# Optimization experiments

Hardware: AMD Instinct MI355X
Metric: run time of the kernel (lower is better)

The kernel has to match this reference:

```python
import jax, jax.numpy as jnp
import numpy as np

N_NODES = 50000
N_EDGES = 600000
IN_DIM = 128
HID_DIM = 128


def setup_inputs() -> dict:
    key = jax.random.key(0)
    k_h, k_src, k_dst, k_w1, k_b1, k_w2, k_b2 = jax.random.split(key, 7)
    h = jax.random.normal(k_h, (N_NODES, IN_DIM), dtype=jnp.float32)
    src = jax.random.randint(k_src, (N_EDGES,), 0, N_NODES, dtype=jnp.int32)
    dst = jax.random.randint(k_dst, (N_EDGES,), 0, N_NODES, dtype=jnp.int32)
    # Edge MLP params: Linear(in_dim, out_dim) -> ReLU -> Linear(out_dim, 1) -> ReLU
    s1 = 1.0 / np.sqrt(IN_DIM)
    s2 = 1.0 / np.sqrt(HID_DIM)
    W1 = jax.random.uniform(k_w1, (IN_DIM, HID_DIM), jnp.float32, -s1, s1)
    b1 = jax.random.uniform(k_b1, (HID_DIM,), jnp.float32, -s1, s1)
    W2 = jax.random.uniform(k_w2, (HID_DIM, 1), jnp.float32, -s2, s2)
    b2 = jax.random.uniform(k_b2, (1,), jnp.float32, -s2, s2)
    return {"h": h, "src": src, "dst": dst, "W1": W1, "b1": b1, "W2": W2, "b2": b2}


def reference(h, src, dst, W1, b1, W2, b2):
    n_nodes = h.shape[0]
    # Edge MLP on feature differences (gather src/dst node features)
    dif = h[src] - h[dst]                                   # [E, D]
    hidden = jax.nn.relu(dif @ W1 + b1)                      # [E, H]
    att = jax.nn.relu(hidden @ W2 + b2)[:, 0]                # [E]
    att = jax.nn.sigmoid(att)                                # [E]
    # EdgeWeightNorm('right') on reversed graph: divide by the sum of
    # attention weights over edges sharing the same ORIGINAL source node.
    denom = jax.ops.segment_sum(att, src, num_segments=n_nodes)  # [N]
    w = att / denom[src]                                     # [E]
    # Message: w_e * src features, sum-aggregated at destination nodes
    msg = w[:, None] * h[src]                                # [E, D]
    out = jax.ops.segment_sum(msg, dst, num_segments=n_nodes)  # [N, D]
    return out
```

## Files before the change

kernel.cpp:

```cpp
#include <hip/hip_runtime.h>


typedef unsigned int uint;
typedef unsigned short ushort;
typedef __attribute__((ext_vector_type(8))) short short8;
typedef __attribute__((ext_vector_type(4))) float f32x4;
typedef __attribute__((ext_vector_type(2))) _Float16 h2;

static __device__ __forceinline__ uint pack_f16(float a, float b) {
  _Float16 ha = (_Float16)a, hb = (_Float16)b;
  unsigned short ua = __builtin_bit_cast(unsigned short, ha);
  unsigned short ub = __builtin_bit_cast(unsigned short, hb);
  return ((uint)ub << 16) | ua;
}
static __device__ __forceinline__ float2 unpack_f16(uint u) {
  _Float16 lo = __builtin_bit_cast(_Float16, (unsigned short)(u & 0xffffu));
  _Float16 hi = __builtin_bit_cast(_Float16, (unsigned short)(u >> 16));
  return make_float2((float)lo, (float)hi);
}
static __device__ __forceinline__ h2 as_h2(uint u) { return __builtin_bit_cast(h2, u); }
static __device__ __forceinline__ h2 relu2(h2 a) {
  h2 r;
  r.x = a.x > (_Float16)0 ? a.x : (_Float16)0;
  r.y = a.y > (_Float16)0 ? a.y : (_Float16)0;
  return r;
}
static __device__ __forceinline__ float dot2acc(h2 a, h2 b, float c) {
#if __has_builtin(__builtin_amdgcn_fdot2)
  return __builtin_amdgcn_fdot2(a, b, c, false);
#else
  return c + (float)a.x * (float)b.x + (float)a.y * (float)b.y;
#endif
}
static __device__ __forceinline__ ushort f2bf(float x) {
  uint u = __float_as_uint(x);
  u += 0x7fffu + ((u >> 16) & 1u);
  return (ushort)(u >> 16);
}

__global__ __launch_bounds__(256) void k_misc(const float* __restrict__ W1,
                                              ushort* __restrict__ w1t_swz,
                                              const int* __restrict__ dst,
                                              int* __restrict__ counts, int n_edges) {
  int b = blockIdx.x;
  if (b < 64) {
    int idx = b * 256 + threadIdx.x;
    int n = idx >> 7, k = idx & 127;
    float v = W1[k * 128 + n];
    int byte_off = n * 256 + ((k * 2) ^ ((n & 7) << 4));
    w1t_swz[byte_off >> 1] = f2bf(v);
  } else {
    int i = (b - 64) * 256 + threadIdx.x;
    int stride = (gridDim.x - 64) * 256;
    for (int e = i; e < n_edges; e += stride) atomicAdd(&counts[dst[e]], 1);
  }
}

__global__ __launch_bounds__(256) void k_gemm(const float* __restrict__ h,
                                              const ushort* __restrict__ w1t_swz,
                                              uint* __restrict__ gh,
                                              uint4* __restrict__ hh4,
                                              int n_nodes) {
  __shared__ ushort w1s[16384];
  int tid = threadIdx.x;
  {
    const uint4* srcw = (const uint4*)w1t_swz;
    uint4* dstw = (uint4*)w1s;
    #pragma unroll
    for (int i = 0; i < 8; ++i) dstw[tid + 256 * i] = srcw[tid + 256 * i];
  }
  __syncthreads();
  int wave = tid >> 6, lane = tid & 63;
  int tile = blockIdx.x * 4 + wave;
  if (tile * 16 >= n_nodes) return;
  int n0 = tile * 16;
  int l15 = lane & 15, kq = lane >> 4;
  int row = n0 + l15;

  f32x4 acc[8];
  #pragma unroll
  for (int ct = 0; ct < 8; ++ct) acc[ct] = (f32x4){0.f, 0.f, 0.f, 0.f};

  #pragma unroll
  for (int kb = 0; kb < 4; ++kb) {
    const float* hp = &h[(size_t)row * 128 + kb * 32 + kq * 8];
    float4 p0 = *(const float4*)hp;
    float4 p1 = *(const float4*)(hp + 4);
    short8 a;
    a[0] = (short)f2bf(p0.x); a[1] = (short)f2bf(p0.y);
    a[2] = (short)f2bf(p0.z); a[3] = (short)f2bf(p0.w);
    a[4] = (short)f2bf(p1.x); a[5] = (short)f2bf(p1.y);
    a[6] = (short)f2bf(p1.z); a[7] = (short)f2bf(p1.w);
    uint4 hv;
    hv.x = pack_f16(p0.x, p0.y); hv.y = pack_f16(p0.z, p0.w);
    hv.z = pack_f16(p1.x, p1.y); hv.w = pack_f16(p1.z, p1.w);
    hh4[(size_t)row * 16 + kb * 4 + kq] = hv;
    #pragma unroll
    for (int ct = 0; ct < 8; ++ct) {
      int n = ct * 16 + l15;
      int byte_off = n * 256 + (((kb * 64) + kq * 16) ^ ((n & 7) << 4));
      short8 b = *(const short8*)((const char*)w1s + byte_off);
      acc[ct] = __builtin_amdgcn_mfma_f32_16x16x32_bf16(a, b, acc[ct], 0, 0, 0);
    }
  }
  ushort* gh16 = (ushort*)gh;
  #pragma unroll
  for (int ct = 0; ct < 8; ++ct) {
    #pragma unroll
    for (int r = 0; r < 4; ++r) {
      int orow = n0 + kq * 4 + r;
      _Float16 v = (_Float16)acc[ct][r];
      gh16[(size_t)orow * 128 + ct * 16 + l15] = __builtin_bit_cast(unsigned short, v);
    }
  }
}

__global__ __launch_bounds__(256) void k_scanA(const int* __restrict__ counts,
                                               int* __restrict__ partials,
                                               int n, int chunk) {
  __shared__ int red[256];
  int b = blockIdx.x, t = threadIdx.x;
  int idx = b * chunk + t;
  red[t] = (t < chunk && idx < n) ? counts[idx] : 0;
  __syncthreads();
  for (int off = 128; off > 0; off >>= 1) {
    if (t < off) red[t] += red[t + off];
    __syncthreads();
  }
  if (t == 0) partials[b] = red[0];
}

__global__ __launch_bounds__(256) void k_scanB(int* __restrict__ partials,
                                               int* __restrict__ row_start,
                                               int n, int total) {
  __shared__ int p[256];
  int t = threadIdx.x;
  int orig = partials[t];
  p[t] = orig;
  __syncthreads();
  #pragma unroll
  for (int off = 1; off < 256; off <<= 1) {
    int v = (t >= off) ? p[t - off] : 0;
    __syncthreads();
    p[t] += v;
    __syncthreads();
  }
  partials[t] = p[t] - orig;
  if (t == 0) row_start[n] = total;
}

__global__ __launch_bounds__(256) void k_scanC(int* __restrict__ counts,
                                               const int* __restrict__ partials,
                                               int* __restrict__ row_start,
                                               int n, int chunk) {
  __shared__ int p[256];
  int b = blockIdx.x, t = threadIdx.x;
  int idx = b * chunk + t;
  bool ok = (t < chunk && idx < n);
  int orig = ok ? counts[idx] : 0;
  p[t] = orig;
  __syncthreads();
  #pragma unroll
  for (int off = 1; off < 256; off <<= 1) {
    int v = (t >= off) ? p[t - off] : 0;
    __syncthreads();
    p[t] += v;
    __syncthreads();
  }
  if (ok) {
    row_start[idx] = partials[b] + p[t] - orig;
    counts[idx] = 0;
  }
}

__global__ __launch_bounds__(256) void k_fill0(const int* __restrict__ src,
                                               const int* __restrict__ dst,
                                               const int* __restrict__ row_start,
                                               int* __restrict__ cursor,
                                               int* __restrict__ bsrc,
                                               int n_edges) {
  int i = blockIdx.x * blockDim.x + threadIdx.x;
  int stride = gridDim.x * blockDim.x;
  for (int e = i; e < n_edges; e += stride) {
    int d = dst[e];
    int pos = atomicAdd(&cursor[d], 1);
    bsrc[row_start[d] + pos] = src[e];
  }
}

__global__ __launch_bounds__(256) void k_att2(const uint4* __restrict__ gh4,
                                              const int* __restrict__ bsrc,
                                              const int* __restrict__ row_start,
                                              const float* __restrict__ b1,
                                              const float* __restrict__ W2,
                                              const float* __restrict__ b2,
                                              int2* __restrict__ bucket,
                                              float* __restrict__ denom,
                                              int n_nodes) {
  int lane = threadIdx.x & 63;
  int sub = lane >> 4, l16 = lane & 15;
  int d = blockIdx.x * 4 + (threadIdx.x >> 6);
  if (d >= n_nodes) return;
  int beg = row_start[d], end = row_start[d + 1];
  if (beg == end) return;
  float4 b1a = *(const float4*)&b1[l16 * 8];
  float4 b1b = *(const float4*)&b1[l16 * 8 + 4];
  float4 w2a = *(const float4*)&W2[l16 * 8];
  float4 w2b = *(const float4*)&W2[l16 * 8 + 4];
  float b2v = b2[0];
  uint4 ud = gh4[(size_t)d * 16 + l16];
  float2 d0 = unpack_f16(ud.x), d1 = unpack_f16(ud.y);
  float2 d2 = unpack_f16(ud.z), d3 = unpack_f16(ud.w);
  h2 c0, c1, c2, c3, wh0, wh1, wh2, wh3;
  c0.x = (_Float16)(b1a.x - d0.x); c0.y = (_Float16)(b1a.y - d0.y);
  c1.x = (_Float16)(b1a.z - d1.x); c1.y = (_Float16)(b1a.w - d1.y);
  c2.x = (_Float16)(b1b.x - d2.x); c2.y = (_Float16)(b1b.y - d2.y);
  c3.x = (_Float16)(b1b.z - d3.x); c3.y = (_Float16)(b1b.w - d3.y);
  wh0.x = (_Float16)w2a.x; wh0.y = (_Float16)w2a.y;
  wh1.x = (_Float16)w2a.z; wh1.y = (_Float16)w2a.w;
  wh2.x = (_Float16)w2b.x; wh2.y = (_Float16)w2b.y;
  wh3.x = (_Float16)w2b.z; wh3.y = (_Float16)w2b.w;
  for (int jb = beg; jb < end; jb += 4) {
    int j = jb + sub;
    bool valid = j < end;
    int s = 0;
    float acc = 0.f;
    if (valid) {
      s = bsrc[j];
      uint4 us = gh4[(size_t)s * 16 + l16];
      acc = dot2acc(relu2(as_h2(us.x) + c0), wh0, acc);
      acc = dot2acc(relu2(as_h2(us.y) + c1), wh1, acc);
      acc = dot2acc(relu2(as_h2(us.z) + c2), wh2, acc);
      acc = dot2acc(relu2(as_h2(us.w) + c3), wh3, acc);
    }
    acc += __shfl_xor(acc, 1);
    acc += __shfl_xor(acc, 2);
    acc += __shfl_xor(acc, 4);
    acc += __shfl_xor(acc, 8);
    if (l16 == 0 && valid) {
      float a = fmaxf(acc + b2v, 0.f);
      a = 1.f / (1.f + __expf(-a));
      bucket[j] = make_int2(s, __float_as_int(a));
      atomicAdd(&denom[s], a);
    }
  }
}

__global__ __launch_bounds__(256) void k_agg(const uint4* __restrict__ hh4,
                                             const int* __restrict__ row_start,
                                             const int2* __restrict__ bucket,
                                             const float* __restrict__ denom,
                                             float* __restrict__ out, int n_nodes) {
  int lane = threadIdx.x & 63;
  int sub = lane >> 4, l16 = lane & 15;
  int d = blockIdx.x * 4 + (threadIdx.x >> 6);
  if (d >= n_nodes) return;
  int beg = row_start[d], end = row_start[d + 1];
  int cnt = end - beg;
  float a0 = 0.f, a1 = 0.f, a2 = 0.f, a3 = 0.f;
  float a4 = 0.f, a5 = 0.f, a6 = 0.f, a7 = 0.f;
  for (int base = 0; base < cnt; base += 64) {
    int nb = cnt - base; if (nb > 64) nb = 64;
    int2 ew = make_int2(0, 0);
    if (lane < nb) {
      ew = bucket[beg + base + lane];
      float w = __int_as_float(ew.y) / denom[ew.x];
      ew.y = __float_as_int(w);
    }
    int steps = (nb + 3) >> 2;
    for (int j = 0; j < steps; ++j) {
      int idx = j * 4 + sub;
      int s = __shfl(ew.x, idx);
      float w = __int_as_float(__shfl(ew.y, idx));
      if (idx < nb) {
        uint4 v = hh4[(size_t)s * 16 + l16];
        float2 f0 = unpack_f16(v.x), f1 = unpack_f16(v.y);
        float2 f2 = unpack_f16(v.z), f3 = unpack_f16(v.w);
        a0 = fmaf(w, f0.x, a0); a1 = fmaf(w, f0.y, a1);
        a2 = fmaf(w, f1.x, a2); a3 = fmaf(w, f1.y, a3);
        a4 = fmaf(w, f2.x, a4); a5 = fmaf(w, f2.y, a5);
        a6 = fmaf(w, f3.x, a6); a7 = fmaf(w, f3.y, a7);
      }
    }
  }
  #pragma unroll
  for (int off = 16; off < 64; off <<= 1) {
    a0 += __shfl_xor(a0, off); a1 += __shfl_xor(a1, off);
    a2 += __shfl_xor(a2, off); a3 += __shfl_xor(a3, off);
    a4 += __shfl_xor(a4, off); a5 += __shfl_xor(a5, off);
    a6 += __shfl_xor(a6, off); a7 += __shfl_xor(a7, off);
  }
  if (sub == 0) {
    *(float4*)&out[(size_t)d * 128 + l16 * 8]     = make_float4(a0, a1, a2, a3);
    *(float4*)&out[(size_t)d * 128 + l16 * 8 + 4] = make_float4(a4, a5, a6, a7);
  }
}

extern "C" void kernel_launch(void* const* d_in, const int* in_sizes, int n_in,
                              void* d_out, int out_size, void* d_ws, size_t ws_size,
                              hipStream_t stream) {
  const float* h   = (const float*)d_in[0];
  const int*   src = (const int*)d_in[1];
  const int*   dst = (const int*)d_in[2];
  const float* W1  = (const float*)d_in[3];
  const float* b1  = (const float*)d_in[4];
  const float* W2  = (const float*)d_in[5];
  const float* b2  = (const float*)d_in[6];
  float* out = (float*)d_out;

  int n_nodes = in_sizes[0] / 128;
  int n_edges = in_sizes[1];

  char* ws = (char*)d_ws;
  uint*   gh        = (uint*)ws;
  uint*   hh        = gh + (size_t)n_nodes * 64;
  float*  denom     = (float*)(hh + (size_t)n_nodes * 64);
  int*    counts    = (int*)(denom + n_nodes);
  int*    row_start = counts + n_nodes;
  int*    partials  = row_start + n_nodes + 1;
  ushort* w1t       = (ushort*)(partials + 256);
  int*    bsrc      = (int*)(w1t + 16384);
  int2*   bucket    = (int2*)(((uintptr_t)(bsrc + n_edges) + 15) & ~(uintptr_t)15);

  hipMemsetAsync(denom, 0, (size_t)2 * n_nodes * sizeof(float), stream);

  int chunk = (n_nodes + 255) / 256;
  int n_tiles = (n_nodes + 15) / 16;
  int nblk4 = (n_nodes + 3) / 4;
  k_misc <<<64 + 1024, 256, 0, stream>>>(W1, w1t, dst, counts, n_edges);
  k_gemm <<<(n_tiles + 3) / 4, 256, 0, stream>>>(h, w1t, gh, (uint4*)hh, n_nodes);
  k_scanA<<<256, 256, 0, stream>>>(counts, partials, n_nodes, chunk);
  k_scanB<<<1, 256, 0, stream>>>(partials, row_start, n_nodes, n_edges);
  k_scanC<<<256, 256, 0, stream>>>(counts, partials, row_start, n_nodes, chunk);
  k_fill0<<<1024, 256, 0, stream>>>(src, dst, row_start, counts, bsrc, n_edges);
  k_att2 <<<nblk4, 256, 0, stream>>>((const uint4*)gh, bsrc, row_start, b1, W2, b2,
                                     bucket, denom, n_nodes);
  k_agg  <<<nblk4, 256, 0, stream>>>((const uint4*)hh, row_start, bucket, denom, out, n_nodes);
}
```

Baseline: 159.3 us.

## Fold memset into prep kernel, overlap dst histogram with GEMM, unroll edge loops

Replaces the hipMemsetAsync of denom/counts with zeroing inside the W1 transpose kernel. The dst-degree histogram atomics move into extra blocks of the GEMM launch so they run alongside the GEMM tiles. The attention and aggregation edge loops are unrolled by two so each lane issues two independent gathers before consuming them. This trades a memset and a launch gap for more register pressure, and relies on the extra histogram blocks sharing the GPU with the shared-memory-heavy GEMM blocks.

```diff
diff --git a/kernel.cpp b/kernel.cpp
--- a/kernel.cpp
+++ b/kernel.cpp
@@ -38,10 +38,9 @@
   return (ushort)(u >> 16);
 }
 
-__global__ __launch_bounds__(256) void k_misc(const float* __restrict__ W1,
+__global__ __launch_bounds__(256) void k_prep(const float* __restrict__ W1,
                                               ushort* __restrict__ w1t_swz,
-                                              const int* __restrict__ dst,
-                                              int* __restrict__ counts, int n_edges) {
+                                              int* __restrict__ zbase, int zwords) {
   int b = blockIdx.x;
   if (b < 64) {
     int idx = b * 256 + threadIdx.x;
@@ -52,7 +51,7 @@
   } else {
     int i = (b - 64) * 256 + threadIdx.x;
     int stride = (gridDim.x - 64) * 256;
-    for (int e = i; e < n_edges; e += stride) atomicAdd(&counts[dst[e]], 1);
+    for (; i < zwords; i += stride) zbase[i] = 0;
   }
 }
 
@@ -60,7 +59,17 @@
                                               const ushort* __restrict__ w1t_swz,
                                               uint* __restrict__ gh,
                                               uint4* __restrict__ hh4,
-                                              int n_nodes) {
+                                              int n_nodes,
+                                              const int* __restrict__ dst,
+                                              int* __restrict__ counts,
+                                              int n_edges, int gemm_blocks) {
+  if ((int)blockIdx.x >= gemm_blocks) {
+    int hb = blockIdx.x - gemm_blocks;
+    int i = hb * 256 + threadIdx.x;
+    int stride = (gridDim.x - gemm_blocks) * 256;
+    for (int e = i; e < n_edges; e += stride) atomicAdd(&counts[dst[e]], 1);
+    return;
+  }
   __shared__ ushort w1s[16384];
   int tid = threadIdx.x;
   {
@@ -220,28 +229,45 @@
   wh1.x = (_Float16)w2a.z; wh1.y = (_Float16)w2a.w;
   wh2.x = (_Float16)w2b.x; wh2.y = (_Float16)w2b.y;
   wh3.x = (_Float16)w2b.z; wh3.y = (_Float16)w2b.w;
-  for (int jb = beg; jb < end; jb += 4) {
-    int j = jb + sub;
-    bool valid = j < end;
-    int s = 0;
-    float acc = 0.f;
-    if (valid) {
-      s = bsrc[j];
-      uint4 us = gh4[(size_t)s * 16 + l16];
-      acc = dot2acc(relu2(as_h2(us.x) + c0), wh0, acc);
-      acc = dot2acc(relu2(as_h2(us.y) + c1), wh1, acc);
-      acc = dot2acc(relu2(as_h2(us.z) + c2), wh2, acc);
-      acc = dot2acc(relu2(as_h2(us.w) + c3), wh3, acc);
-    }
-    acc += __shfl_xor(acc, 1);
-    acc += __shfl_xor(acc, 2);
-    acc += __shfl_xor(acc, 4);
-    acc += __shfl_xor(acc, 8);
-    if (l16 == 0 && valid) {
-      float a = fmaxf(acc + b2v, 0.f);
-      a = 1.f / (1.f + __expf(-a));
-      bucket[j] = make_int2(s, __float_as_int(a));
-      atomicAdd(&denom[s], a);
+  for (int jb = beg; jb < end; jb += 8) {
+    int j0 = jb + sub, j1 = jb + sub + 4;
+    bool v0 = j0 < end, v1 = j1 < end;
+    int s0 = 0, s1 = 0;
+    float acc0 = 0.f, acc1 = 0.f;
+    if (v0) s0 = bsrc[j0];
+    if (v1) s1 = bsrc[j1];
+    uint4 ua, ub;
+    if (v0) ua = gh4[(size_t)s0 * 16 + l16];
+    if (v1) ub = gh4[(size_t)s1 * 16 + l16];
+    if (v0) {
+      acc0 = dot2acc(relu2(as_h2(ua.x) + c0), wh0, acc0);
+      acc0 = dot2acc(relu2(as_h2(ua.y) + c1), wh1, acc0);
+      acc0 = dot2acc(relu2(as_h2(ua.z) + c2), wh2, acc0);
+      acc0 = dot2acc(relu2(as_h2(ua.w) + c3), wh3, acc0);
+    }
+    if (v1) {
+      acc1 = dot2acc(relu2(as_h2(ub.x) + c0), wh0, acc1);
+      acc1 = dot2acc(relu2(as_h2(ub.y) + c1), wh1, acc1);
+      acc1 = dot2acc(relu2(as_h2(ub.z) + c2), wh2, acc1);
+      acc1 = dot2acc(relu2(as_h2(ub.w) + c3), wh3, acc1);
+    }
+    acc0 += __shfl_xor(acc0, 1); acc1 += __shfl_xor(acc1, 1);
+    acc0 += __shfl_xor(acc0, 2); acc1 += __shfl_xor(acc1, 2);
+    acc0 += __shfl_xor(acc0, 4); acc1 += __shfl_xor(acc1, 4);
+    acc0 += __shfl_xor(acc0, 8); acc1 += __shfl_xor(acc1, 8);
+    if (l16 == 0) {
+      if (v0) {
+        float a = fmaxf(acc0 + b2v, 0.f);
+        a = 1.f / (1.f + __expf(-a));
+        bucket[j0] = make_int2(s0, __float_as_int(a));
+        atomicAdd(&denom[s0], a);
+      }
+      if (v1) {
+        float a = fmaxf(acc1 + b2v, 0.f);
+        a = 1.f / (1.f + __expf(-a));
+        bucket[j1] = make_int2(s1, __float_as_int(a));
+        atomicAdd(&denom[s1], a);
+      }
     }
   }
 }
@@ -268,18 +294,45 @@
       ew.y = __float_as_int(w);
     }
     int steps = (nb + 3) >> 2;
-    for (int j = 0; j < steps; ++j) {
-      int idx = j * 4 + sub;
-      int s = __shfl(ew.x, idx);
-      float w = __int_as_float(__shfl(ew.y, idx));
-      if (idx < nb) {
-        uint4 v = hh4[(size_t)s * 16 + l16];
-        float2 f0 = unpack_f16(v.x), f1 = unpack_f16(v.y);
-        float2 f2 = unpack_f16(v.z), f3 = unpack_f16(v.w);
-        a0 = fmaf(w, f0.x, a0); a1 = fmaf(w, f0.y, a1);
-        a2 = fmaf(w, f1.x, a2); a3 = fmaf(w, f1.y, a3);
-        a4 = fmaf(w, f2.x, a4); a5 = fmaf(w, f2.y, a5);
-        a6 = fmaf(w, f3.x, a6); a7 = fmaf(w, f3.y, a7);
+    int jj = 0;
+    for (; jj + 2 <= steps; jj += 2) {
+      int i0 = jj * 4 + sub, i1 = i0 + 4;
+      int sA = __shfl(ew.x, i0), sB = __shfl(ew.x, i1);
+      float wA = __int_as_float(__shfl(ew.y, i0));
+      float wB = __int_as_float(__shfl(ew.y, i1));
+      bool vA = i0 < nb, vB = i1 < nb;
+      uint4 va, vb;
+      if (vA) va = hh4[(size_t)sA * 16 + l16];
+      if (vB) vb = hh4[(size_t)sB * 16 + l16];
+      if (vA) {
+        float2 f0 = unpack_f16(va.x), f1 = unpack_f16(va.y);
+        float2 f2 = unpack_f16(va.z), f3 = unpack_f16(va.w);
+        a0 = fmaf(wA, f0.x, a0); a1 = fmaf(wA, f0.y, a1);
+        a2 = fmaf(wA, f1.x, a2); a3 = fmaf(wA, f1.y, a3);
+        a4 = fmaf(wA, f2.x, a4); a5 = fmaf(wA, f2.y, a5);
+        a6 = fmaf(wA, f3.x, a6); a7 = fmaf(wA, f3.y, a7);
+      }
+      if (vB) {
+        float2 f0 = unpack_f16(vb.x), f1 = unpack_f16(vb.y);
+        float2 f2 = unpack_f16(vb.z), f3 = unpack_f16(vb.w);
+        a0 = fmaf(wB, f0.x, a0); a1 = fmaf(wB, f0.y, a1);
+        a2 = fmaf(wB, f1.x, a2); a3 = fmaf(wB, f1.y, a3);
+        a4 = fmaf(wB, f2.x, a4); a5 = fmaf(wB, f2.y, a5);
+        a6 = fmaf(wB, f3.x, a6); a7 = fmaf(wB, f3.y, a7);
+      }
+    }
+    if (jj < steps) {
+      int i0 = jj * 4 + sub;
+      int sA = __shfl(ew.x, i0);
+      float wA = __int_as_float(__shfl(ew.y, i0));
+      if (i0 < nb) {
+        uint4 va = hh4[(size_t)sA * 16 + l16];
+        float2 f0 = unpack_f16(va.x), f1 = unpack_f16(va.y);
+        float2 f2 = unpack_f16(va.z), f3 = unpack_f16(va.w);
+        a0 = fmaf(wA, f0.x, a0); a1 = fmaf(wA, f0.y, a1);
+        a2 = fmaf(wA, f1.x, a2); a3 = fmaf(wA, f1.y, a3);
+        a4 = fmaf(wA, f2.x, a4); a5 = fmaf(wA, f2.y, a5);
+        a6 = fmaf(wA, f3.x, a6); a7 = fmaf(wA, f3.y, a7);
       }
     }
   }
@@ -322,13 +375,13 @@
   int*    bsrc      = (int*)(w1t + 16384);
   int2*   bucket    = (int2*)(((uintptr_t)(bsrc + n_edges) + 15) & ~(uintptr_t)15);
 
-  hipMemsetAsync(denom, 0, (size_t)2 * n_nodes * sizeof(float), stream);
-
   int chunk = (n_nodes + 255) / 256;
   int n_tiles = (n_nodes + 15) / 16;
+  int gemm_blocks = (n_tiles + 3) / 4;
   int nblk4 = (n_nodes + 3) / 4;
-  k_misc <<<64 + 1024, 256, 0, stream>>>(W1, w1t, dst, counts, n_edges);
-  k_gemm <<<(n_tiles + 3) / 4, 256, 0, stream>>>(h, w1t, gh, (uint4*)hh, n_nodes);
+  k_prep <<<64 + 16, 256, 0, stream>>>(W1, w1t, (int*)denom, 2 * n_nodes);
+  k_gemm <<<gemm_blocks + 256, 256, 0, stream>>>(h, w1t, gh, (uint4*)hh, n_nodes,
+                                                 dst, counts, n_edges, gemm_blocks);
   k_scanA<<<256, 256, 0, stream>>>(counts, partials, n_nodes, chunk);
   k_scanB<<<1, 256, 0, stream>>>(partials, row_start, n_nodes, n_edges);
   k_scanC<<<256, 256, 0, stream>>>(counts, partials, row_start, n_nodes, chunk);
```

Result: faster. 155.6 us (-2.3%).
